# Kernel optimization log

Hardware: AMD Instinct MI355X
Metric: run time of the kernel (lower is better)

## Reference

```python
import jax, jax.numpy as jnp
import numpy as np

THRESHOLD = 0.6
SCALE = 1.0


def _tffix(mat):
    # floor for >=0, ceil for <0 (round toward zero)
    return jnp.where(mat >= 0, jnp.floor(mat), jnp.ceil(mat))


def _rec2square(rect):
    # rect: [N,5] = x1,y1,x2,y2,score -> square boxes, same center-ish rule as original
    x1, y1, x2, y2, s = rect[:, 0], rect[:, 1], rect[:, 2], rect[:, 3], rect[:, 4]
    w = x2 - x1
    h = y2 - y1
    l = jnp.maximum(w, h)
    nx1 = x1 + w * 0.5 - l * 0.5
    ny1 = y1 + h * 0.5 - l * 0.5
    return jnp.stack([nx1, ny1, nx1 + l, ny1 + l, s], axis=-1)


def _post_single(cls_el, roi_el):
    # cls_el: [H,W,2], roi_el: [H,W,4]
    H, W = cls_el.shape[0], cls_el.shape[1]
    # Cls_pro = transpose(classifier[...,1:2], [1,0,2]) -> prob[w,h]
    prob = cls_el[:, :, 1].T                      # [W,H]
    roi = jnp.transpose(roi_el, (2, 1, 0))        # [4,W,H]
    out_side = max(W, H)                          # static shapes -> python scalar
    stride = ((2 * out_side + 11 - 12) / (out_side - 1)) if (2 * out_side != 11) else 0.0
    stride = jnp.float32(stride)
    # all grid positions in row-major order over [W,H] (matches tf.where ordering)
    wi, hi = jnp.meshgrid(jnp.arange(W), jnp.arange(H), indexing='ij')
    bb = jnp.stack([wi, hi], axis=-1).astype(jnp.float32).reshape(-1, 2)   # [WH,2]
    bb1 = _tffix(stride * bb)
    bb2 = _tffix(stride * bb + 11.0)
    offset = roi.reshape(4, -1).T                 # [WH,4] = dx1..dx4 per position
    box = jnp.concatenate([bb1, bb2], axis=-1) + offset * 12.0 * SCALE      # [WH,4]
    score = prob.reshape(-1, 1)                   # [WH,1]
    rect = _rec2square(jnp.concatenate([box, score], axis=-1))              # [WH,5]
    # fixed-shape compaction of the tf.where(prob>=thr) selection:
    mask = prob.reshape(-1) >= THRESHOLD
    order = jnp.argsort(jnp.logical_not(mask), stable=True)  # valid rows first, stable
    rect = rect[order] * mask[order][:, None].astype(rect.dtype)            # pad rows = 0
    return rect


def setup_inputs() -> dict:
    key = jax.random.key(0)
    k1, k2 = jax.random.split(key)
    B, H, W = 16, 540, 960
    classifier = jax.random.uniform(k1, (B, H, W, 2), dtype=jnp.float32)
    bbox_regress = jax.random.normal(k2, (B, H, W, 4), dtype=jnp.float32)
    img_shape = jnp.ones((B, 2), dtype=jnp.float32)
    return {"classifier": classifier, "bbox_regress": bbox_regress, "img_shape": img_shape}


def reference(classifier, bbox_regress, img_shape):
    rect = jax.vmap(_post_single)(classifier, bbox_regress)   # [B, H*W, 5]
    return (rect, rect, img_shape + 1.0)
```

## Files before the change

### kernel.cpp

```cpp
#include <hip/hip_runtime.h>

#define HH 540
#define WW 960
#define NB 16
#define NPB (HH * WW)
#define NF  (NPB * 5)
static const float STRIDE_F = (float)(1919.0 / 959.0);
#define THR 0.6f

__global__ void k_zero(int* __restrict__ p, int n) {
    int i = blockIdx.x * blockDim.x + threadIdx.x;
    if (i < n) p[i] = 0;
}

__global__ void k_count(const float4* __restrict__ cls4, int* __restrict__ colcnt) {
    int tw = blockIdx.x * 256 + threadIdx.x;
    int b = blockIdx.z;
    int h0 = blockIdx.y * 54;
    if (tw >= WW / 2) return;
    int w0 = tw * 2;
    const float4* base = cls4 + (size_t)b * (NPB / 2);
    int c0 = 0, c1 = 0;
    for (int h = h0; h < h0 + 54; ++h) {
        float4 v = base[(size_t)(h * WW + w0) >> 1];
        c0 += (v.y >= THR) ? 1 : 0;
        c1 += (v.w >= THR) ? 1 : 0;
    }
    if (c0) atomicAdd(&colcnt[b * WW + w0], c0);
    if (c1) atomicAdd(&colcnt[b * WW + w0 + 1], c1);
}

__global__ void k_scan(const int* __restrict__ colcnt, int* __restrict__ colbase,
                       int* __restrict__ totals, const float* __restrict__ img,
                       float* __restrict__ out_img) {
    __shared__ int s[1024];
    int b = blockIdx.x;
    int t = threadIdx.x;
    int v = (t < WW) ? colcnt[b * WW + t] : 0;
    s[t] = v;
    __syncthreads();
    for (int d = 1; d < 1024; d <<= 1) {
        int x = s[t];
        int y = (t >= d) ? s[t - d] : 0;
        __syncthreads();
        s[t] = x + y;
        __syncthreads();
    }
    if (t < WW) colbase[b * WW + t] = s[t] - v;
    if (t == 0) totals[b] = s[1023];
    if (t < 2) out_img[b * 2 + t] = img[b * 2 + t] + 1.0f;
}

__global__ __launch_bounds__(256) void k_compact(const float* __restrict__ cls,
                                                 const float4* __restrict__ roi,
                                                 const int* __restrict__ colbase,
                                                 float* __restrict__ out1,
                                                 float* __restrict__ out2) {
    __shared__ int wcnt_s[4][16];
    __shared__ float rows_s[16 * 80];
    int t = threadIdx.x;
    int w_l = t & 15;
    int h_l = t >> 4;
    int wave = t >> 6;
    int h_lw = h_l & 3;
    int b = blockIdx.y;
    int w = blockIdx.x * 16 + w_l;
    const float*  cbase = cls + (size_t)b * NPB * 2;
    const float4* rbase = roi + (size_t)b * NPB;

    int fc = h_l;
    int fj = w_l;
    int cb_f = colbase[b * WW + blockIdx.x * 16 + fc];
    int run_f = 0;

    float sxw = truncf(STRIDE_F * (float)w);
    float exw = truncf(STRIDE_F * (float)w + 11.0f);

    for (int ih = 0; ih < 34; ++ih) {
        int h = ih * 16 + h_l;
        bool valid = h < HH;
        float p = valid ? cbase[(size_t)(h * WW + w) * 2 + 1] : 0.0f;
        bool m = valid && (p >= THR);

        unsigned long long bal = __ballot(m);
        unsigned long long colmask = 0x0001000100010001ULL << w_l;
        int off_w = __popcll(bal & colmask & ((1ULL << (h_lw * 16)) - 1ULL));
        int wc    = __popcll(bal & colmask);

        __syncthreads();
        if (h_lw == 0) wcnt_s[wave][w_l] = wc;
        __syncthreads();

        int off = off_w;
#pragma unroll
        for (int v = 0; v < 4; ++v) {
            int x = wcnt_s[v][w_l];
            if (v < wave) off += x;
        }

        if (m) {
            float4 r = rbase[h * WW + w];
            float sy = truncf(STRIDE_F * (float)h);
            float ey = truncf(STRIDE_F * (float)h + 11.0f);
            float x1 = sxw + r.x * 12.0f;
            float y1 = sy  + r.y * 12.0f;
            float x2 = exw + r.z * 12.0f;
            float y2 = ey  + r.w * 12.0f;
            float wd = x2 - x1;
            float hd = y2 - y1;
            float l  = fmaxf(wd, hd);
            float nx1 = x1 + wd * 0.5f - l * 0.5f;
            float ny1 = y1 + hd * 0.5f - l * 0.5f;
            int sb = w_l * 80 + off * 5;
            rows_s[sb + 0] = nx1;
            rows_s[sb + 1] = ny1;
            rows_s[sb + 2] = nx1 + l;
            rows_s[sb + 3] = ny1 + l;
            rows_s[sb + 4] = p;
        }
        __syncthreads();

        int tot_f = wcnt_s[0][fc] + wcnt_s[1][fc] + wcnt_s[2][fc] + wcnt_s[3][fc];
        int nd = tot_f * 5;
        size_t gb = ((size_t)b * NPB + (size_t)(cb_f + run_f)) * 5;
        for (int d = fj; d < nd; d += 16) {
            float val = rows_s[fc * 80 + d];
            out1[gb + d] = val;
            out2[gb + d] = val;
        }
        run_f += tot_f;
    }
}

__global__ void k_ztail(const int* __restrict__ totals, float* __restrict__ out1,
                        float* __restrict__ out2) {
    int b = blockIdx.y;
    int K5 = totals[b] * 5;
    int chunk = blockIdx.x * blockDim.x + threadIdx.x;
    int f0 = chunk * 4;
    if (f0 >= NF) return;
    size_t base = (size_t)b * NF;
    if (f0 >= K5) {
        float4 z = make_float4(0.f, 0.f, 0.f, 0.f);
        *(float4*)(out1 + base + f0) = z;
        *(float4*)(out2 + base + f0) = z;
    } else if (f0 + 4 > K5) {
        for (int j = K5; j < f0 + 4; ++j) {
            out1[base + j] = 0.0f;
            out2[base + j] = 0.0f;
        }
    }
}

extern "C" void kernel_launch(void* const* d_in, const int* in_sizes, int n_in,
                              void* d_out, int out_size, void* d_ws, size_t ws_size,
                              hipStream_t stream) {
    const float* cls = (const float*)d_in[0];
    const float* roi = (const float*)d_in[1];
    const float* img = (const float*)d_in[2];

    float* out1 = (float*)d_out;
    float* out2 = out1 + (size_t)NB * NF;
    float* outimg = out2 + (size_t)NB * NF;

    int* colcnt  = (int*)d_ws;
    int* colbase = colcnt + NB * WW;
    int* totals  = colbase + NB * WW;

    k_zero<<<dim3((NB * WW + 255) / 256), dim3(256), 0, stream>>>(colcnt, NB * WW);
    k_count<<<dim3(2, 10, NB), dim3(256), 0, stream>>>((const float4*)cls, colcnt);
    k_scan<<<dim3(NB), dim3(1024), 0, stream>>>(colcnt, colbase, totals, img, outimg);
    k_compact<<<dim3(60, NB), dim3(256), 0, stream>>>(cls, (const float4*)roi, colbase,
                                                      out1, out2);
    k_ztail<<<dim3((NF / 4 + 255) / 256, NB), dim3(256), 0, stream>>>(totals, out1, out2);
}
```

Before: 515.8 us.

## Split compaction into per-tile blocks with precomputed per-chunk base offsets

Counting now runs per 16x16 tile and writes per-(row-chunk, column) counts without atomics. The scan turns these into a base offset for each chunk. The compaction kernel then runs one block per tile across a 60x34x16 grid instead of 960 blocks that each loop serially over 34 row chunks, which removes the serial chain of barriers and gives far more parallelism. In exchange it needs more workspace, the scan does more serial work per thread, and the count kernel now reads only the odd floats, which is less coalesced than the earlier float4 loads.

New measurement: 504.1 us. 2.3% less time.

```diff
diff --git a/kernel.cpp b/kernel.cpp
--- a/kernel.cpp
+++ b/kernel.cpp
@@ -3,41 +3,51 @@
 #define HH 540
 #define WW 960
 #define NB 16
+#define NCH 34
 #define NPB (HH * WW)
 #define NF  (NPB * 5)
 static const float STRIDE_F = (float)(1919.0 / 959.0);
 #define THR 0.6f
 
-__global__ void k_zero(int* __restrict__ p, int n) {
-    int i = blockIdx.x * blockDim.x + threadIdx.x;
-    if (i < n) p[i] = 0;
+__global__ __launch_bounds__(256) void k_cnt(const float* __restrict__ cls,
+                                             int* __restrict__ cnt) {
+    __shared__ int wcnt_s[4][16];
+    int t = threadIdx.x;
+    int w_l = t & 15;
+    int h_l = t >> 4;
+    int wave = t >> 6;
+    int h_lw = h_l & 3;
+    int hc = blockIdx.y;
+    int b = blockIdx.z;
+    int w = blockIdx.x * 16 + w_l;
+    int h = hc * 16 + h_l;
+    bool valid = h < HH;
+    const float* cbase = cls + (size_t)b * NPB * 2;
+    float p = valid ? cbase[(size_t)(h * WW + w) * 2 + 1] : 0.0f;
+    bool m = valid && (p >= THR);
+    unsigned long long bal = __ballot(m);
+    unsigned long long colmask = 0x0001000100010001ULL << w_l;
+    int wc = __popcll(bal & colmask);
+    if (h_lw == 0) wcnt_s[wave][w_l] = wc;
+    __syncthreads();
+    if (t < 16) {
+        int tot = wcnt_s[0][t] + wcnt_s[1][t] + wcnt_s[2][t] + wcnt_s[3][t];
+        cnt[((size_t)b * NCH + hc) * WW + blockIdx.x * 16 + t] = tot;
+    }
 }
 
-__global__ void k_count(const float4* __restrict__ cls4, int* __restrict__ colcnt) {
-    int tw = blockIdx.x * 256 + threadIdx.x;
-    int b = blockIdx.z;
-    int h0 = blockIdx.y * 54;
-    if (tw >= WW / 2) return;
-    int w0 = tw * 2;
-    const float4* base = cls4 + (size_t)b * (NPB / 2);
-    int c0 = 0, c1 = 0;
-    for (int h = h0; h < h0 + 54; ++h) {
-        float4 v = base[(size_t)(h * WW + w0) >> 1];
-        c0 += (v.y >= THR) ? 1 : 0;
-        c1 += (v.w >= THR) ? 1 : 0;
-    }
-    if (c0) atomicAdd(&colcnt[b * WW + w0], c0);
-    if (c1) atomicAdd(&colcnt[b * WW + w0 + 1], c1);
-}
-
-__global__ void k_scan(const int* __restrict__ colcnt, int* __restrict__ colbase,
+__global__ void k_scan(const int* __restrict__ cnt, int* __restrict__ abase,
                        int* __restrict__ totals, const float* __restrict__ img,
                        float* __restrict__ out_img) {
     __shared__ int s[1024];
     int b = blockIdx.x;
     int t = threadIdx.x;
-    int v = (t < WW) ? colcnt[b * WW + t] : 0;
-    s[t] = v;
+    const int* c = cnt + (size_t)b * NCH * WW;
+    int tot = 0;
+    if (t < WW) {
+        for (int hc = 0; hc < NCH; ++hc) tot += c[hc * WW + t];
+    }
+    s[t] = tot;
     __syncthreads();
     for (int d = 1; d < 1024; d <<= 1) {
         int x = s[t];
@@ -46,89 +56,87 @@
         s[t] = x + y;
         __syncthreads();
     }
-    if (t < WW) colbase[b * WW + t] = s[t] - v;
+    if (t < WW) {
+        int run = s[t] - tot;
+        int* ab = abase + (size_t)b * NCH * WW;
+        for (int hc = 0; hc < NCH; ++hc) {
+            ab[hc * WW + t] = run;
+            run += c[hc * WW + t];
+        }
+    }
     if (t == 0) totals[b] = s[1023];
     if (t < 2) out_img[b * 2 + t] = img[b * 2 + t] + 1.0f;
 }
 
 __global__ __launch_bounds__(256) void k_compact(const float* __restrict__ cls,
                                                  const float4* __restrict__ roi,
-                                                 const int* __restrict__ colbase,
+                                                 const int* __restrict__ abase,
                                                  float* __restrict__ out1,
                                                  float* __restrict__ out2) {
     __shared__ int wcnt_s[4][16];
-    __shared__ float rows_s[16 * 80];
+    __shared__ float rows_s[16 * 85];
     int t = threadIdx.x;
     int w_l = t & 15;
     int h_l = t >> 4;
     int wave = t >> 6;
     int h_lw = h_l & 3;
-    int b = blockIdx.y;
+    int hc = blockIdx.y;
+    int b = blockIdx.z;
     int w = blockIdx.x * 16 + w_l;
+    int h = hc * 16 + h_l;
     const float*  cbase = cls + (size_t)b * NPB * 2;
     const float4* rbase = roi + (size_t)b * NPB;
 
+    bool valid = h < HH;
+    float p = valid ? cbase[(size_t)(h * WW + w) * 2 + 1] : 0.0f;
+    bool m = valid && (p >= THR);
+
+    unsigned long long bal = __ballot(m);
+    unsigned long long colmask = 0x0001000100010001ULL << w_l;
+    int off = __popcll(bal & colmask & ((1ULL << (h_lw * 16)) - 1ULL));
+    int wc  = __popcll(bal & colmask);
+    if (h_lw == 0) wcnt_s[wave][w_l] = wc;
+    __syncthreads();
+#pragma unroll
+    for (int v = 0; v < 4; ++v) {
+        int x = wcnt_s[v][w_l];
+        if (v < wave) off += x;
+    }
+
+    if (m) {
+        float4 r = rbase[h * WW + w];
+        float sxw = truncf(STRIDE_F * (float)w);
+        float exw = truncf(STRIDE_F * (float)w + 11.0f);
+        float sy  = truncf(STRIDE_F * (float)h);
+        float ey  = truncf(STRIDE_F * (float)h + 11.0f);
+        float x1 = sxw + r.x * 12.0f;
+        float y1 = sy  + r.y * 12.0f;
+        float x2 = exw + r.z * 12.0f;
+        float y2 = ey  + r.w * 12.0f;
+        float wd = x2 - x1;
+        float hd = y2 - y1;
+        float l  = fmaxf(wd, hd);
+        float nx1 = x1 + wd * 0.5f - l * 0.5f;
+        float ny1 = y1 + hd * 0.5f - l * 0.5f;
+        int sb = w_l * 85 + off * 5;
+        rows_s[sb + 0] = nx1;
+        rows_s[sb + 1] = ny1;
+        rows_s[sb + 2] = nx1 + l;
+        rows_s[sb + 3] = ny1 + l;
+        rows_s[sb + 4] = p;
+    }
+    __syncthreads();
+
     int fc = h_l;
     int fj = w_l;
-    int cb_f = colbase[b * WW + blockIdx.x * 16 + fc];
-    int run_f = 0;
-
-    float sxw = truncf(STRIDE_F * (float)w);
-    float exw = truncf(STRIDE_F * (float)w + 11.0f);
-
-    for (int ih = 0; ih < 34; ++ih) {
-        int h = ih * 16 + h_l;
-        bool valid = h < HH;
-        float p = valid ? cbase[(size_t)(h * WW + w) * 2 + 1] : 0.0f;
-        bool m = valid && (p >= THR);
-
-        unsigned long long bal = __ballot(m);
-        unsigned long long colmask = 0x0001000100010001ULL << w_l;
-        int off_w = __popcll(bal & colmask & ((1ULL << (h_lw * 16)) - 1ULL));
-        int wc    = __popcll(bal & colmask);
-
-        __syncthreads();
-        if (h_lw == 0) wcnt_s[wave][w_l] = wc;
-        __syncthreads();
-
-        int off = off_w;
-#pragma unroll
-        for (int v = 0; v < 4; ++v) {
-            int x = wcnt_s[v][w_l];
-            if (v < wave) off += x;
-        }
-
-        if (m) {
-            float4 r = rbase[h * WW + w];
-            float sy = truncf(STRIDE_F * (float)h);
-            float ey = truncf(STRIDE_F * (float)h + 11.0f);
-            float x1 = sxw + r.x * 12.0f;
-            float y1 = sy  + r.y * 12.0f;
-            float x2 = exw + r.z * 12.0f;
-            float y2 = ey  + r.w * 12.0f;
-            float wd = x2 - x1;
-            float hd = y2 - y1;
-            float l  = fmaxf(wd, hd);
-            float nx1 = x1 + wd * 0.5f - l * 0.5f;
-            float ny1 = y1 + hd * 0.5f - l * 0.5f;
-            int sb = w_l * 80 + off * 5;
-            rows_s[sb + 0] = nx1;
-            rows_s[sb + 1] = ny1;
-            rows_s[sb + 2] = nx1 + l;
-            rows_s[sb + 3] = ny1 + l;
-            rows_s[sb + 4] = p;
-        }
-        __syncthreads();
-
-        int tot_f = wcnt_s[0][fc] + wcnt_s[1][fc] + wcnt_s[2][fc] + wcnt_s[3][fc];
-        int nd = tot_f * 5;
-        size_t gb = ((size_t)b * NPB + (size_t)(cb_f + run_f)) * 5;
-        for (int d = fj; d < nd; d += 16) {
-            float val = rows_s[fc * 80 + d];
-            out1[gb + d] = val;
-            out2[gb + d] = val;
-        }
-        run_f += tot_f;
+    int tot_f = wcnt_s[0][fc] + wcnt_s[1][fc] + wcnt_s[2][fc] + wcnt_s[3][fc];
+    int cb_f = abase[((size_t)b * NCH + hc) * WW + blockIdx.x * 16 + fc];
+    int nd = tot_f * 5;
+    size_t gb = ((size_t)b * NPB + (size_t)cb_f) * 5;
+    for (int d = fj; d < nd; d += 16) {
+        float val = rows_s[fc * 85 + d];
+        out1[gb + d] = val;
+        out2[gb + d] = val;
     }
 }
 
@@ -163,14 +171,13 @@
     float* out2 = out1 + (size_t)NB * NF;
     float* outimg = out2 + (size_t)NB * NF;
 
-    int* colcnt  = (int*)d_ws;
-    int* colbase = colcnt + NB * WW;
-    int* totals  = colbase + NB * WW;
+    int* cnt    = (int*)d_ws;
+    int* abase  = cnt + (size_t)NB * NCH * WW;
+    int* totals = abase + (size_t)NB * NCH * WW;
 
-    k_zero<<<dim3((NB * WW + 255) / 256), dim3(256), 0, stream>>>(colcnt, NB * WW);
-    k_count<<<dim3(2, 10, NB), dim3(256), 0, stream>>>((const float4*)cls, colcnt);
-    k_scan<<<dim3(NB), dim3(1024), 0, stream>>>(colcnt, colbase, totals, img, outimg);
-    k_compact<<<dim3(60, NB), dim3(256), 0, stream>>>(cls, (const float4*)roi, colbase,
-                                                      out1, out2);
+    k_cnt<<<dim3(60, NCH, NB), dim3(256), 0, stream>>>(cls, cnt);
+    k_scan<<<dim3(NB), dim3(1024), 0, stream>>>(cnt, abase, totals, img, outimg);
+    k_compact<<<dim3(60, NCH, NB), dim3(256), 0, stream>>>(cls, (const float4*)roi,
+                                                           abase, out1, out2);
     k_ztail<<<dim3((NF / 4 + 255) / 256, NB), dim3(256), 0, stream>>>(totals, out1, out2);
 }
```
